# Performance work log

Measured on AMD Instinct MI355X. Metric: run time of the kernel, lower is better.

The kernel has to match this reference:

```python
import jax, jax.numpy as jnp
import numpy as np

N_NODES = 32768
N_EDGES = 524288
IN_CH = 128
OUT_CH = 128
EDGE_CH = 64
HIDDEN = 128


def setup_inputs() -> dict:
    key = jax.random.key(0)
    ks = jax.random.split(key, 8)
    x = jax.random.normal(ks[0], (N_NODES, IN_CH), dtype=jnp.float32)
    edge_index = jax.random.randint(ks[1], (2, N_EDGES), 0, N_NODES, dtype=jnp.int64)
    edge_attr = jax.random.uniform(ks[2], (N_EDGES, EDGE_CH), dtype=jnp.float32)
    # filter_network: Linear(edge_ch, hidden) -> tanh -> Linear(hidden, out)
    s1 = 1.0 / np.sqrt(EDGE_CH)
    s2 = 1.0 / np.sqrt(HIDDEN)
    W1 = jax.random.uniform(ks[3], (EDGE_CH, HIDDEN), jnp.float32, -s1, s1)
    b1 = jax.random.uniform(ks[4], (HIDDEN,), jnp.float32, -s1, s1)
    W2 = jax.random.uniform(ks[5], (HIDDEN, OUT_CH), jnp.float32, -s2, s2)
    b2 = jax.random.uniform(ks[6], (OUT_CH,), jnp.float32, -s2, s2)
    # attention_vector [out, 1], xavier_uniform with gain 1.414
    lim = 1.414 * np.sqrt(6.0 / (OUT_CH + 1))
    attn = jax.random.uniform(ks[7], (OUT_CH,), jnp.float32, -lim, lim)
    return {"x": x, "edge_index": edge_index, "edge_attr": edge_attr,
            "W1": W1, "b1": b1, "W2": W2, "b2": b2, "attn": attn}


def _segment_softmax(scores, segment_ids, num_segments):
    # PyG-style numerically stable softmax over segments
    seg_max = jax.ops.segment_max(scores, segment_ids, num_segments=num_segments)
    seg_max = jnp.where(jnp.isfinite(seg_max), seg_max, 0.0)
    e = jnp.exp(scores - seg_max[segment_ids])
    denom = jax.ops.segment_sum(e, segment_ids, num_segments=num_segments)
    return e / (denom[segment_ids] + 1e-16)


def reference(x, edge_index, edge_attr, W1, b1, W2, b2, attn):
    source, target = edge_index[0], edge_index[1]
    n_nodes = x.shape[0]
    source_features = x[source]                                  # [E, in]
    edge_attr_norm = edge_attr / (jnp.linalg.norm(edge_attr, axis=-1, keepdims=True) + 1e-8)
    h = jnp.tanh(edge_attr_norm @ W1 + b1)                       # [E, hidden]
    edge_filters = h @ W2 + b2                                   # [E, out]
    messages = source_features * edge_filters                    # [E, out]
    attention_scores = messages @ attn                           # [E]
    attention_weights = _segment_softmax(attention_scores, target, n_nodes)
    messages = messages * attention_weights[:, None]
    output = jax.ops.segment_sum(messages, target, num_segments=n_nodes)  # [N, out]
    return output, attention_weights
```

## Files before the change

### kernel.cpp

```cpp
#include <hip/hip_runtime.h>
#include <stdint.h>

typedef short short8 __attribute__((ext_vector_type(8)));
typedef float f32x16 __attribute__((ext_vector_type(16)));
typedef unsigned ux4 __attribute__((ext_vector_type(4)));

__device__ __forceinline__ unsigned cvtpk(float lo, float hi){
  unsigned r;
  asm("v_cvt_pk_bf16_f32 %0, %1, %2" : "=v"(r) : "v"(lo), "v"(hi));
  return r;
}

__device__ __forceinline__ short8 frag_from(unsigned a, unsigned b, unsigned c, unsigned d){
  union { unsigned u[4]; short8 s; } t;
  t.u[0] = a; t.u[1] = b; t.u[2] = c; t.u[3] = d;
  return t.s;
}

__global__ void k_prep(const float* __restrict__ W1, const float* __restrict__ W2,
                       ux4* __restrict__ Wf)
{
  const int t = blockIdx.x * 256 + threadIdx.x;
  if (t >= 48 * 64) return;
  const int f = t >> 6, l = t & 63;
  const int r = l & 31, hh = l >> 5;
  float v[8];
  if (f < 16) {
    const int mf = f >> 2, ks = f & 3;
    const int c = 32 * mf + r, kb = ks * 16 + hh * 8;
#pragma unroll
    for (int j = 0; j < 8; ++j) v[j] = W1[(kb + j) * 128 + c];
  } else {
    const int f2 = f - 16, mf2 = f2 >> 3, ks = f2 & 7;
    const int o = 32 * mf2 + r, cb = ks * 16 + hh * 8;
#pragma unroll
    for (int j = 0; j < 8; ++j) v[j] = W2[(cb + j) * 128 + o];
  }
  ux4 d;
  d.x = cvtpk(v[0], v[1]); d.y = cvtpk(v[2], v[3]);
  d.z = cvtpk(v[4], v[5]); d.w = cvtpk(v[6], v[7]);
  Wf[(long long)f * 64 + l] = d;
}

__global__ void k_setup(const float* __restrict__ x, uint2* __restrict__ xb, int n4,
                        const int* __restrict__ ei, int* __restrict__ rowptr, int E)
{
  const long long tot = (n4 > E) ? n4 : E;
  for (long long i = (long long)blockIdx.x * 256 + threadIdx.x; i < tot;
       i += (long long)gridDim.x * 256) {
    if (i < n4) {
      float4 v = ((const float4*)x)[i];
      uint2 o; o.x = cvtpk(v.x, v.y); o.y = cvtpk(v.z, v.w);
      xb[i] = o;
    }
    if (i < E) atomicAdd(&rowptr[ei[E + i]], 1);
  }
}

__global__ __launch_bounds__(1024)
void k_scan(int* __restrict__ p, int N){
  __shared__ int ls[1024];
  const int t = threadIdx.x;
  const int chunk = (N + 1023) >> 10;
  const int c0 = t * chunk, c1 = min(N, c0 + chunk);
  int s = 0;
  for (int i = c0; i < c1; ++i) s += p[i];
  ls[t] = s;
  __syncthreads();
  for (int off = 1; off < 1024; off <<= 1) {
    int add = (t >= off) ? ls[t - off] : 0;
    __syncthreads();
    ls[t] += add;
    __syncthreads();
  }
  int run = (t == 0) ? 0 : ls[t - 1];
  for (int i = c0; i < c1; ++i) { int v = p[i]; p[i] = run; run += v; }
}

__global__ void k_fill(const int* __restrict__ ei, int* __restrict__ rowptr,
                       int* __restrict__ pose, int* __restrict__ eidx, int E){
  for (long long i = (long long)blockIdx.x * 256 + threadIdx.x; i < E;
       i += (long long)gridDim.x * 256) {
    int tg = ei[E + i];
    int pos = atomicAdd(&rowptr[tg], 1);
    pose[i] = pos;
    eidx[pos] = (int)i;
  }
}

#define K1B 512
__global__ __launch_bounds__(K1B)
void k1_fused(const unsigned* __restrict__ xb, const int* __restrict__ ei,
              const float* __restrict__ ea, const ux4* __restrict__ Wf,
              const float* __restrict__ b1, const float* __restrict__ b2,
              const float* __restrict__ attn, const int* __restrict__ eidx,
              unsigned* __restrict__ msgp, float* __restrict__ scoreS, int E)
{
  __shared__ ux4 sWf[48 * 64];
  for (int i = threadIdx.x; i < 48 * 64; i += K1B) sWf[i] = Wf[i];
  __syncthreads();

  const int lane = threadIdx.x & 63;
  const int wv   = threadIdx.x >> 6;
  const int h    = lane >> 5;
  const int r31  = lane & 31;
  const long long gstep = (long long)gridDim.x * (K1B / 64) * 32;
  long long p = ((long long)blockIdx.x * (K1B / 64) + wv) * 32 + r31;
  if (p - r31 >= E) return;

  int eC = eidx[(p < E) ? p : (long long)(E - 1)];
  int srcC = ei[eC];
  unsigned ebC[4][4]; float rinC;
  {
    const float* er = ea + (long long)eC * 64 + h * 8;
    float4 v[8];
#pragma unroll
    for (int ks = 0; ks < 4; ++ks) {
      v[2*ks]   = *(const float4*)(er + ks * 16);
      v[2*ks+1] = *(const float4*)(er + ks * 16 + 4);
    }
    float ss = 0.f;
#pragma unroll
    for (int k8 = 0; k8 < 8; ++k8) {
      ss = fmaf(v[k8].x, v[k8].x, ss); ss = fmaf(v[k8].y, v[k8].y, ss);
      ss = fmaf(v[k8].z, v[k8].z, ss); ss = fmaf(v[k8].w, v[k8].w, ss);
    }
    ss += __shfl_xor(ss, 32);
    rinC = 1.0f / (sqrtf(ss) + 1e-8f);
#pragma unroll
    for (int ks = 0; ks < 4; ++ks) {
      ebC[ks][0] = cvtpk(v[2*ks].x,   v[2*ks].y);
      ebC[ks][1] = cvtpk(v[2*ks].z,   v[2*ks].w);
      ebC[ks][2] = cvtpk(v[2*ks+1].x, v[2*ks+1].y);
      ebC[ks][3] = cvtpk(v[2*ks+1].z, v[2*ks+1].w);
    }
  }
  long long pn = p + gstep;
  bool hasN = (pn - r31) < E;
  int eN = 0;
  if (hasN) eN = eidx[(pn < E) ? pn : (long long)(E - 1)];

  while (true) {
    float4 eaN[8]; int srcN = 0;
    if (hasN) {
      srcN = ei[eN];
      const float* er = ea + (long long)eN * 64 + h * 8;
#pragma unroll
      for (int ks = 0; ks < 4; ++ks) {
        eaN[2*ks]   = *(const float4*)(er + ks * 16);
        eaN[2*ks+1] = *(const float4*)(er + ks * 16 + 4);
      }
    }
    long long pnn = pn + gstep;
    bool hasNN = hasN && ((pnn - r31) < E);
    int eNN = 0;
    if (hasNN) eNN = eidx[(pnn < E) ? pnn : (long long)(E - 1)];

    const unsigned* xrow = xb + (long long)srcC * 64;
    uint2 xw[4];
#pragma unroll
    for (int rq = 0; rq < 4; ++rq)
      xw[rq] = *(const uint2*)(xrow + (8*rq + 4*h) / 2);
    asm volatile("" ::: "memory");

    unsigned hb[8][4];
#pragma unroll
    for (int mf = 0; mf < 4; ++mf) {
      f32x16 a1;
#pragma unroll
      for (int i = 0; i < 16; ++i) a1[i] = 0.f;
#pragma unroll
      for (int ks = 0; ks < 4; ++ks) {
        ux4 w = sWf[(mf * 4 + ks) * 64 + lane];
        a1 = __builtin_amdgcn_mfma_f32_32x32x16_bf16(
            frag_from(w.x, w.y, w.z, w.w),
            frag_from(ebC[ks][0], ebC[ks][1], ebC[ks][2], ebC[ks][3]), a1, 0, 0, 0);
      }
      float hv[16];
#pragma unroll
      for (int rq = 0; rq < 4; ++rq) {
        float4 bc = *(const float4*)(b1 + 32*mf + 8*rq + 4*h);
#pragma unroll
        for (int i = 0; i < 4; ++i) {
          float pre = fmaf(a1[rq*4+i], rinC, ((const float*)&bc)[i]);
          float e2  = __expf(2.0f * pre);
          hv[rq*4+i] = 1.0f - 2.0f / (e2 + 1.0f);
        }
      }
#pragma unroll
      for (int q = 0; q < 2; ++q) {
        unsigned A = cvtpk(hv[q*8+0], hv[q*8+1]);
        unsigned B = cvtpk(hv[q*8+2], hv[q*8+3]);
        unsigned C = cvtpk(hv[q*8+4], hv[q*8+5]);
        unsigned D = cvtpk(hv[q*8+6], hv[q*8+7]);
        unsigned Axr = (unsigned)__shfl_xor((int)A, 32);
        unsigned Bxr = (unsigned)__shfl_xor((int)B, 32);
        unsigned Cxr = (unsigned)__shfl_xor((int)C, 32);
        unsigned Dxr = (unsigned)__shfl_xor((int)D, 32);
        hb[2*mf+q][0] = h ? Cxr : A;
        hb[2*mf+q][1] = h ? Dxr : B;
        hb[2*mf+q][2] = h ? C   : Axr;
        hb[2*mf+q][3] = h ? D   : Bxr;
      }
    }

    float score = 0.f;
#pragma unroll
    for (int mf2 = 0; mf2 < 4; ++mf2) {
      uint2 xwN[4];
      if (mf2 < 3) {
#pragma unroll
        for (int rq = 0; rq < 4; ++rq)
          xwN[rq] = *(const uint2*)(xrow + (32*(mf2+1) + 8*rq + 4*h) / 2);
      }
      f32x16 a2;
#pragma unroll
      for (int i = 0; i < 16; ++i) a2[i] = 0.f;
#pragma unroll
      for (int ks = 0; ks < 8; ++ks) {
        ux4 w = sWf[(16 + mf2 * 8 + ks) * 64 + lane];
        a2 = __builtin_amdgcn_mfma_f32_32x32x16_bf16(
            frag_from(w.x, w.y, w.z, w.w),
            frag_from(hb[ks][0], hb[ks][1], hb[ks][2], hb[ks][3]), a2, 0, 0, 0);
      }
      unsigned pk[8];
#pragma unroll
      for (int rq = 0; rq < 4; ++rq) {
        const int o0 = 32*mf2 + 8*rq + 4*h;
        float4 b2c = *(const float4*)(b2 + o0);
        float4 atc = *(const float4*)(attn + o0);
        float x0 = __uint_as_float(xw[rq].x << 16);
        float x1 = __uint_as_float(xw[rq].x & 0xffff0000u);
        float x2 = __uint_as_float(xw[rq].y << 16);
        float x3 = __uint_as_float(xw[rq].y & 0xffff0000u);
        float m0 = (a2[rq*4+0] + b2c.x) * x0;
        float m1 = (a2[rq*4+1] + b2c.y) * x1;
        float m2 = (a2[rq*4+2] + b2c.z) * x2;
        float m3 = (a2[rq*4+3] + b2c.w) * x3;
        score = fmaf(m0, atc.x, score);
        score = fmaf(m1, atc.y, score);
        score = fmaf(m2, atc.z, score);
        score = fmaf(m3, atc.w, score);
        pk[2*rq]   = cvtpk(m0, m1);
        pk[2*rq+1] = cvtpk(m2, m3);
      }
      if (p < E) {
        ux4* dst = (ux4*)(msgp + p * 64 + 16*mf2 + 8*h);
        ux4 s0, s1;
        s0.x = pk[0]; s0.y = pk[1]; s0.z = pk[2]; s0.w = pk[3];
        s1.x = pk[4]; s1.y = pk[5]; s1.z = pk[6]; s1.w = pk[7];
        dst[0] = s0; dst[1] = s1;
      }
      if (mf2 < 3) {
#pragma unroll
        for (int rq = 0; rq < 4; ++rq) xw[rq] = xwN[rq];
      }
    }
    score += __shfl_xor(score, 32);
    if (h == 0 && p < E) scoreS[p] = score;

    if (!hasN) break;
    float ss = 0.f;
#pragma unroll
    for (int k8 = 0; k8 < 8; ++k8) {
      ss = fmaf(eaN[k8].x, eaN[k8].x, ss); ss = fmaf(eaN[k8].y, eaN[k8].y, ss);
      ss = fmaf(eaN[k8].z, eaN[k8].z, ss); ss = fmaf(eaN[k8].w, eaN[k8].w, ss);
    }
    ss += __shfl_xor(ss, 32);
    rinC = 1.0f / (sqrtf(ss) + 1e-8f);
#pragma unroll
    for (int ks = 0; ks < 4; ++ks) {
      ebC[ks][0] = cvtpk(eaN[2*ks].x,   eaN[2*ks].y);
      ebC[ks][1] = cvtpk(eaN[2*ks].z,   eaN[2*ks].w);
      ebC[ks][2] = cvtpk(eaN[2*ks+1].x, eaN[2*ks+1].y);
      ebC[ks][3] = cvtpk(eaN[2*ks+1].z, eaN[2*ks+1].w);
    }
    srcC = srcN; p = pn; pn = pnn; hasN = hasNN; eN = eNN;
  }
}

__global__ __launch_bounds__(256)
void k_gather(const unsigned* __restrict__ msgp, const float* __restrict__ scoreS,
              const int* __restrict__ rowptr, float* __restrict__ lse,
              float* __restrict__ out, int N)
{
  const int lane = threadIdx.x & 63;
  const int node = blockIdx.x * 4 + (threadIdx.x >> 6);
  if (node >= N) return;
  const int end   = rowptr[node];
  const int start = node ? rowptr[node - 1] : 0;
  const int L     = end - start;

  float m = -3.4e38f, s = 0.f;
  for (int c0 = 0; c0 < L; c0 += 64) {
    const int j = c0 + lane;
    float sc = (j < L) ? scoreS[start + j] : -3.4e38f;
    float cm = sc;
#pragma unroll
    for (int off = 32; off; off >>= 1) cm = fmaxf(cm, __shfl_xor(cm, off));
    const float mn = fmaxf(m, cm);
    float ex = (j < L) ? __expf(sc - mn) : 0.f;
#pragma unroll
    for (int off = 32; off; off >>= 1) ex += __shfl_xor(ex, off);
    s = s * __expf(m - mn) + ex;
    m = mn;
  }
  const float lsev = m + logf(s + 1e-16f);
  if (lane == 0) lse[node] = lsev;

  float2 acc; acc.x = 0.f; acc.y = 0.f;
  for (int c0 = 0; c0 < L; c0 += 64) {
    const int j = c0 + lane;
    float w = (j < L) ? __expf(scoreS[start + j] - lsev) : 0.f;
    const int jn = min(64, L - c0);
#pragma unroll 4
    for (int j2 = 0; j2 < jn; ++j2) {
      float wj = __shfl(w, j2);
      unsigned md = msgp[(long long)(start + c0 + j2) * 64 + lane];
      acc.x = fmaf(wj, __uint_as_float(md << 16),          acc.x);
      acc.y = fmaf(wj, __uint_as_float(md & 0xffff0000u), acc.y);
    }
  }
  const int mf2 = lane >> 4, hh = (lane >> 3) & 1, rq = (lane >> 1) & 3, half = lane & 1;
  const int ch0 = 32*mf2 + 8*rq + 4*hh + 2*half;
  *(float2*)(out + (long long)node * 128 + ch0) = acc;
}

__global__ void k_wfin(int* __restrict__ pw, const int* __restrict__ ei,
                       const float* __restrict__ scoreS, const float* __restrict__ lse,
                       int E){
  for (long long i = (long long)blockIdx.x * 256 + threadIdx.x; i < E;
       i += (long long)gridDim.x * 256) {
    int pos = pw[i];
    float w = __expf(scoreS[pos] - lse[ei[E + i]]);
    pw[i] = __float_as_int(w);
  }
}

extern "C" void kernel_launch(void* const* d_in, const int* in_sizes, int n_in,
                              void* d_out, int out_size, void* d_ws, size_t ws_size,
                              hipStream_t stream)
{
  const float* x    = (const float*)d_in[0];
  const int*   ei   = (const int*)d_in[1];
  const float* ea   = (const float*)d_in[2];
  const float* W1   = (const float*)d_in[3];
  const float* b1   = (const float*)d_in[4];
  const float* W2   = (const float*)d_in[5];
  const float* b2   = (const float*)d_in[6];
  const float* attn = (const float*)d_in[7];
  const int N = in_sizes[0] / 128;
  const int E = in_sizes[2] / 64;
  if (E <= 0 || N <= 0) return;

  float* out   = (float*)d_out;
  float* wregN = out + (long long)N * 128;
  ux4*     Wf   = (ux4*)d_out;
  size_t   offE = 65536;
  int*     eidx = (int*)((char*)d_out + offE);
  size_t   offX = (offE + (size_t)E * 4 + 255) & ~(size_t)255;
  unsigned* xb  = (unsigned*)((char*)d_out + offX);

  char* wsb = (char*)d_ws;
  unsigned* msgp   = (unsigned*)wsb;
  float*    scoreS = (float*)(wsb + (size_t)E * 256);
  int*      rowptr = (int*)(wsb + (size_t)E * 256 + (size_t)E * 4);
  float*    lse    = (float*)(wsb + (size_t)E * 260 + (size_t)N * 4);
  const size_t need = (size_t)E * 260 + (size_t)N * 8;
  if (ws_size < need) return;
  if ((size_t)out_size < (size_t)N * 128 + (size_t)E) return;
  if ((size_t)N * 512 < offX + (size_t)N * 256) return;

  (void)hipMemsetAsync(rowptr, 0, (size_t)N * 4, stream);
  k_prep<<<12, 256, 0, stream>>>(W1, W2, Wf);
  k_setup<<<1024, 256, 0, stream>>>(x, (uint2*)xb, N * 32, ei, rowptr, E);
  k_scan<<<1, 1024, 0, stream>>>(rowptr, N);
  k_fill<<<1024, 256, 0, stream>>>(ei, rowptr, (int*)wregN, eidx, E);
  const long long nwaves = ((long long)E + 31) / 32;
  const int grid = (int)min((long long)512, (nwaves + (K1B/64) - 1) / (K1B/64));
  k1_fused<<<grid, K1B, 0, stream>>>(xb, ei, ea, Wf, b1, b2, attn,
                                     eidx, msgp, scoreS, E);
  k_gather<<<(N + 3) / 4, 256, 0, stream>>>(msgp, scoreS, rowptr, lse, out, N);
  k_wfin<<<1024, 256, 0, stream>>>((int*)wregN, ei, scoreS, lse, E);
}
```

Before: 277.8 us.

## Fuse weight finalization into gather and merge weight prep into setup

Merges the W1/W2 fragment-prep kernel into the setup kernel, removing one launch. When workspace is large enough, eidx lives in workspace and the gather kernel scatters normalized attention weights directly to their original edge positions, eliminating the k_wfin pass and the pose array. Adds a single-pass softmax fast path for nodes with at most 64 incoming edges. Scattered weight writes are uncoalesced, and which path runs depends on the workspace size.

Measured after the change: 267.6 us. 3.6% less time.

```diff
diff --git a/kernel.cpp b/kernel.cpp
--- a/kernel.cpp
+++ b/kernel.cpp
@@ -17,37 +17,34 @@
   return t.s;
 }
 
-__global__ void k_prep(const float* __restrict__ W1, const float* __restrict__ W2,
-                       ux4* __restrict__ Wf)
+__global__ void k_setup(const float* __restrict__ x, uint2* __restrict__ xb, int n4,
+                        const int* __restrict__ ei, int* __restrict__ rowptr, int E,
+                        const float* __restrict__ W1, const float* __restrict__ W2,
+                        ux4* __restrict__ Wf)
 {
-  const int t = blockIdx.x * 256 + threadIdx.x;
-  if (t >= 48 * 64) return;
-  const int f = t >> 6, l = t & 63;
-  const int r = l & 31, hh = l >> 5;
-  float v[8];
-  if (f < 16) {
-    const int mf = f >> 2, ks = f & 3;
-    const int c = 32 * mf + r, kb = ks * 16 + hh * 8;
-#pragma unroll
-    for (int j = 0; j < 8; ++j) v[j] = W1[(kb + j) * 128 + c];
-  } else {
-    const int f2 = f - 16, mf2 = f2 >> 3, ks = f2 & 7;
-    const int o = 32 * mf2 + r, cb = ks * 16 + hh * 8;
-#pragma unroll
-    for (int j = 0; j < 8; ++j) v[j] = W2[(cb + j) * 128 + o];
-  }
-  ux4 d;
-  d.x = cvtpk(v[0], v[1]); d.y = cvtpk(v[2], v[3]);
-  d.z = cvtpk(v[4], v[5]); d.w = cvtpk(v[6], v[7]);
-  Wf[(long long)f * 64 + l] = d;
-}
-
-__global__ void k_setup(const float* __restrict__ x, uint2* __restrict__ xb, int n4,
-                        const int* __restrict__ ei, int* __restrict__ rowptr, int E)
-{
+  const long long tid = (long long)blockIdx.x * 256 + threadIdx.x;
+  if (tid < 48 * 64) {
+    const int f = (int)(tid >> 6), l = (int)(tid & 63);
+    const int r = l & 31, hh = l >> 5;
+    float v[8];
+    if (f < 16) {
+      const int mf = f >> 2, ks = f & 3;
+      const int c = 32 * mf + r, kb = ks * 16 + hh * 8;
+#pragma unroll
+      for (int j = 0; j < 8; ++j) v[j] = W1[(kb + j) * 128 + c];
+    } else {
+      const int f2 = f - 16, mf2 = f2 >> 3, ks = f2 & 7;
+      const int o = 32 * mf2 + r, cb = ks * 16 + hh * 8;
+#pragma unroll
+      for (int j = 0; j < 8; ++j) v[j] = W2[(cb + j) * 128 + o];
+    }
+    ux4 d;
+    d.x = cvtpk(v[0], v[1]); d.y = cvtpk(v[2], v[3]);
+    d.z = cvtpk(v[4], v[5]); d.w = cvtpk(v[6], v[7]);
+    Wf[(long long)f * 64 + l] = d;
+  }
   const long long tot = (n4 > E) ? n4 : E;
-  for (long long i = (long long)blockIdx.x * 256 + threadIdx.x; i < tot;
-       i += (long long)gridDim.x * 256) {
+  for (long long i = tid; i < tot; i += (long long)gridDim.x * 256) {
     if (i < n4) {
       float4 v = ((const float4*)x)[i];
       uint2 o; o.x = cvtpk(v.x, v.y); o.y = cvtpk(v.z, v.w);
@@ -83,7 +80,7 @@
        i += (long long)gridDim.x * 256) {
     int tg = ei[E + i];
     int pos = atomicAdd(&rowptr[tg], 1);
-    pose[i] = pos;
+    if (pose) pose[i] = pos;
     eidx[pos] = (int)i;
   }
 }
@@ -279,9 +276,11 @@
   }
 }
 
+template<int FUSEW>
 __global__ __launch_bounds__(256)
 void k_gather(const unsigned* __restrict__ msgp, const float* __restrict__ scoreS,
-              const int* __restrict__ rowptr, float* __restrict__ lse,
+              const int* __restrict__ rowptr, const int* __restrict__ eidx,
+              float* __restrict__ lse, float* __restrict__ wreg,
               float* __restrict__ out, int N)
 {
   const int lane = threadIdx.x & 63;
@@ -291,34 +290,60 @@
   const int start = node ? rowptr[node - 1] : 0;
   const int L     = end - start;
 
-  float m = -3.4e38f, s = 0.f;
-  for (int c0 = 0; c0 < L; c0 += 64) {
-    const int j = c0 + lane;
-    float sc = (j < L) ? scoreS[start + j] : -3.4e38f;
-    float cm = sc;
-#pragma unroll
-    for (int off = 32; off; off >>= 1) cm = fmaxf(cm, __shfl_xor(cm, off));
-    const float mn = fmaxf(m, cm);
-    float ex = (j < L) ? __expf(sc - mn) : 0.f;
-#pragma unroll
-    for (int off = 32; off; off >>= 1) ex += __shfl_xor(ex, off);
-    s = s * __expf(m - mn) + ex;
-    m = mn;
-  }
-  const float lsev = m + logf(s + 1e-16f);
-  if (lane == 0) lse[node] = lsev;
-
   float2 acc; acc.x = 0.f; acc.y = 0.f;
-  for (int c0 = 0; c0 < L; c0 += 64) {
-    const int j = c0 + lane;
-    float w = (j < L) ? __expf(scoreS[start + j] - lsev) : 0.f;
-    const int jn = min(64, L - c0);
+
+  if (L <= 64) {
+    float sc = (lane < L) ? scoreS[start + lane] : -3.4e38f;
+    float mn = sc;
+#pragma unroll
+    for (int off = 32; off; off >>= 1) mn = fmaxf(mn, __shfl_xor(mn, off));
+    float ex = (lane < L) ? __expf(sc - mn) : 0.f;
+    float s = ex;
+#pragma unroll
+    for (int off = 32; off; off >>= 1) s += __shfl_xor(s, off);
+    const float w = ex / (s + 1e-16f);
+    if (FUSEW) {
+      if (lane < L) wreg[eidx[start + lane]] = w;
+    } else if (lane == 0) {
+      lse[node] = mn + logf(s + 1e-16f);
+    }
 #pragma unroll 4
-    for (int j2 = 0; j2 < jn; ++j2) {
+    for (int j2 = 0; j2 < L; ++j2) {
       float wj = __shfl(w, j2);
-      unsigned md = msgp[(long long)(start + c0 + j2) * 64 + lane];
+      unsigned md = msgp[(long long)(start + j2) * 64 + lane];
       acc.x = fmaf(wj, __uint_as_float(md << 16),          acc.x);
       acc.y = fmaf(wj, __uint_as_float(md & 0xffff0000u), acc.y);
+    }
+  } else {
+    float m = -3.4e38f, s = 0.f;
+    for (int c0 = 0; c0 < L; c0 += 64) {
+      const int j = c0 + lane;
+      float sc = (j < L) ? scoreS[start + j] : -3.4e38f;
+      float cm = sc;
+#pragma unroll
+      for (int off = 32; off; off >>= 1) cm = fmaxf(cm, __shfl_xor(cm, off));
+      const float mn = fmaxf(m, cm);
+      float ex = (j < L) ? __expf(sc - mn) : 0.f;
+#pragma unroll
+      for (int off = 32; off; off >>= 1) ex += __shfl_xor(ex, off);
+      s = s * __expf(m - mn) + ex;
+      m = mn;
+    }
+    const float lsev = m + logf(s + 1e-16f);
+    if (!FUSEW && lane == 0) lse[node] = lsev;
+
+    for (int c0 = 0; c0 < L; c0 += 64) {
+      const int j = c0 + lane;
+      float w = (j < L) ? __expf(scoreS[start + j] - lsev) : 0.f;
+      if (FUSEW && j < L) wreg[eidx[start + j]] = w;
+      const int jn = min(64, L - c0);
+#pragma unroll 4
+      for (int j2 = 0; j2 < jn; ++j2) {
+        float wj = __shfl(w, j2);
+        unsigned md = msgp[(long long)(start + c0 + j2) * 64 + lane];
+        acc.x = fmaf(wj, __uint_as_float(md << 16),          acc.x);
+        acc.y = fmaf(wj, __uint_as_float(md & 0xffff0000u), acc.y);
+      }
     }
   }
   const int mf2 = lane >> 4, hh = (lane >> 3) & 1, rq = (lane >> 1) & 3, half = lane & 1;
@@ -355,31 +380,41 @@
 
   float* out   = (float*)d_out;
   float* wregN = out + (long long)N * 128;
-  ux4*     Wf   = (ux4*)d_out;
-  size_t   offE = 65536;
-  int*     eidx = (int*)((char*)d_out + offE);
-  size_t   offX = (offE + (size_t)E * 4 + 255) & ~(size_t)255;
-  unsigned* xb  = (unsigned*)((char*)d_out + offX);
+  ux4*     Wf     = (ux4*)d_out;
+  size_t   offE   = 65536;
+  int*     eidxDO = (int*)((char*)d_out + offE);
+  size_t   offX   = (offE + (size_t)E * 4 + 255) & ~(size_t)255;
+  unsigned* xb    = (unsigned*)((char*)d_out + offX);
 
   char* wsb = (char*)d_ws;
   unsigned* msgp   = (unsigned*)wsb;
   float*    scoreS = (float*)(wsb + (size_t)E * 256);
-  int*      rowptr = (int*)(wsb + (size_t)E * 256 + (size_t)E * 4);
+  int*      rowptr = (int*)(wsb + (size_t)E * 260);
   float*    lse    = (float*)(wsb + (size_t)E * 260 + (size_t)N * 4);
-  const size_t need = (size_t)E * 260 + (size_t)N * 8;
-  if (ws_size < need) return;
+  int*      eidxWS = (int*)(wsb + (size_t)E * 260 + (size_t)N * 8);
+  const size_t need1 = (size_t)E * 260 + (size_t)N * 8;
+  const size_t need2 = need1 + (size_t)E * 4;
+  if (ws_size < need1) return;
   if ((size_t)out_size < (size_t)N * 128 + (size_t)E) return;
   if ((size_t)N * 512 < offX + (size_t)N * 256) return;
 
+  const bool fused = (ws_size >= need2);
+  int* eidx = fused ? eidxWS : eidxDO;
+
   (void)hipMemsetAsync(rowptr, 0, (size_t)N * 4, stream);
-  k_prep<<<12, 256, 0, stream>>>(W1, W2, Wf);
-  k_setup<<<1024, 256, 0, stream>>>(x, (uint2*)xb, N * 32, ei, rowptr, E);
+  k_setup<<<1024, 256, 0, stream>>>(x, (uint2*)xb, N * 32, ei, rowptr, E, W1, W2, Wf);
   k_scan<<<1, 1024, 0, stream>>>(rowptr, N);
-  k_fill<<<1024, 256, 0, stream>>>(ei, rowptr, (int*)wregN, eidx, E);
+  k_fill<<<1024, 256, 0, stream>>>(ei, rowptr, fused ? nullptr : (int*)wregN, eidx, E);
   const long long nwaves = ((long long)E + 31) / 32;
   const int grid = (int)min((long long)512, (nwaves + (K1B/64) - 1) / (K1B/64));
   k1_fused<<<grid, K1B, 0, stream>>>(xb, ei, ea, Wf, b1, b2, attn,
                                      eidx, msgp, scoreS, E);
-  k_gather<<<(N + 3) / 4, 256, 0, stream>>>(msgp, scoreS, rowptr, lse, out, N);
-  k_wfin<<<1024, 256, 0, stream>>>((int*)wregN, ei, scoreS, lse, E);
-}
+  if (fused) {
+    k_gather<1><<<(N + 3) / 4, 256, 0, stream>>>(msgp, scoreS, rowptr, eidx,
+                                                 lse, wregN, out, N);
+  } else {
+    k_gather<0><<<(N + 3) / 4, 256, 0, stream>>>(msgp, scoreS, rowptr, eidx,
+                                                 lse, wregN, out, N);
+    k_wfin<<<1024, 256, 0, stream>>>((int*)wregN, ei, scoreS, lse, E);
+  }
+}
```
